# Optimization experiments

Measured on AMD Instinct MI355X. Metric: run time of the kernel, lower is better.

The kernel has to match this reference:

```python
import jax, jax.numpy as jnp
import numpy as np

EPS = 1e-5

def group_points(feat, idx):
    # feat: [B, C, N1], idx: [B, N2, K] -> [B, C, N2, K]
    return jax.vmap(lambda f, i: f[:, i])(feat, idx)

def conv_bn_relu(x, W, gamma, beta):
    # 1x1 conv2d (no bias) + training-mode BatchNorm2d + ReLU
    y = jnp.einsum('oc,bcnk->bonk', W, x)
    mean = y.mean(axis=(0, 2, 3), keepdims=True)
    var = y.var(axis=(0, 2, 3), keepdims=True)  # biased, as BN uses for normalization
    y = (y - mean) * jax.lax.rsqrt(var + EPS)
    y = y * gamma[None, :, None, None] + beta[None, :, None, None]
    return jax.nn.relu(y)

def setup_inputs() -> dict:
    key = jax.random.key(0)
    ks = jax.random.split(key, 12)
    B, N1, N2, K, C1 = 16, 4096, 1024, 32, 64
    mlp = [C1 + 3, 64, 64, 128]  # use_xyz adds 3 channels
    inp = {
        'in_xyz': jax.random.normal(ks[0], (B, 3, N1), jnp.float32),
        'out_xyz': jax.random.normal(ks[1], (B, 3, N2), jnp.float32),
        'in_feature': jax.random.normal(ks[2], (B, C1, N1), jnp.float32),
        'nbr_index': jax.random.randint(ks[3], (B, N2, K), 0, N1, jnp.int32),
    }
    for li in range(3):
        cin, cout = mlp[li], mlp[li + 1]
        inp[f'W{li}'] = jax.random.normal(ks[4 + li], (cout, cin), jnp.float32) * (1.0 / np.sqrt(cin))
        inp[f'g{li}'] = jnp.ones((cout,), jnp.float32)
        inp[f'b{li}'] = jnp.zeros((cout,), jnp.float32)
    return inp

def reference(in_xyz, out_xyz, in_feature, nbr_index,
              W0, g0, b0, W1, g1, b1, W2, g2, b2):
    # gather neighbor features: [B, C1, N2, K]
    nbr_feature = group_points(in_feature, nbr_index)
    # gather neighbor xyz, recenter on query points: [B, 3, N2, K]
    nbr_xyz = group_points(in_xyz, nbr_index) - out_xyz[:, :, :, None]
    x = jnp.concatenate([nbr_feature, nbr_xyz], axis=1)  # [B, C1+3, N2, K]
    x = conv_bn_relu(x, W0, g0, b0)
    x = conv_bn_relu(x, W1, g1, b1)
    x = conv_bn_relu(x, W2, g2, b2)
    return jnp.max(x, axis=3)  # [B, C2, N2]
```

## Files before the change

### kernel.cpp

```cpp
#include <hip/hip_runtime.h>
#include <cstdint>

typedef unsigned short u16;
typedef unsigned int   u32;
typedef __attribute__((ext_vector_type(8))) short  short8;
typedef __attribute__((ext_vector_type(4))) float  floatx4;

#define NPTS 524288

__device__ __forceinline__ float b2f(u16 h) { return __uint_as_float(((u32)h) << 16); }
__device__ __forceinline__ u16 f2b(float f) {
  u32 u = __float_as_uint(f);
  return (u16)((u + 0x7FFFu + ((u >> 16) & 1u)) >> 16);
}
__device__ __forceinline__ u32 pk_bf16(float lo, float hi) {
  return (u32)f2b(lo) | ((u32)f2b(hi) << 16);
}
__device__ __forceinline__ short8 ld_frag8(const u16* p) {
  union { uint4 q; short8 s; } x;
  x.q = *(const uint4*)p;
  return x.s;
}
__device__ __forceinline__ void bar_lds() {
  asm volatile("s_waitcnt lgkmcnt(0)\n\ts_barrier" ::: "memory");
}

__global__ __launch_bounds__(256) void prep_all(const float* __restrict__ inf,
                                                const float* __restrict__ ixyz,
                                                const float* __restrict__ W0,
                                                const float* __restrict__ W1,
                                                const float* __restrict__ W2,
                                                u16* __restrict__ featT,
                                                float4* __restrict__ xyzT,
                                                u16* __restrict__ Wb) {
  __shared__ float tile[32 * 33];
  const int bk = blockIdx.x, t = threadIdx.x;
  if (bk < 4096) {
    int b = bk >> 8, rem = bk & 255, cc = rem >> 7, nc = rem & 127;
    #pragma unroll
    for (int i = 0; i < 4; ++i) {
      int flat = t + i * 256;
      int cl = flat >> 5, nl = flat & 31;
      tile[cl * 33 + nl] = inf[(size_t)((b * 64) + cc * 32 + cl) * 4096 + nc * 32 + nl];
    }
    __syncthreads();
    #pragma unroll
    for (int i = 0; i < 4; ++i) {
      int flat = t + i * 256;
      int nl = flat >> 5, cl = flat & 31;
      featT[(size_t)((b << 12) + nc * 32 + nl) * 64 + cc * 32 + cl] = f2b(tile[cl * 33 + nl]);
    }
  } else if (bk < 4352) {
    int g = (bk - 4096) * 256 + t;
    int b = g >> 12, n = g & 4095;
    const float* p = ixyz + (size_t)b * 12288;
    xyzT[g] = make_float4(p[n], p[4096 + n], p[8192 + n], 0.f);
  } else {
    int s = (bk - 4352) * 256 + t;
    u16 v = 0;
    if (s < 6656)       { int o = s / 104, c = s % 104; if (c < 67) v = f2b(W0[o * 67 + c]); }
    else if (s < 11264) { int q = s - 6656;  int o = q / 72, c = q % 72; if (c < 64) v = f2b(W1[o * 64 + c]); }
    else                { int q = s - 11264; int o = q / 72, c = q % 72; if (c < 64) v = f2b(W2[o * 64 + c]); }
    Wb[s] = v;
  }
}

template<int KSTEPS, int OCH, bool GATHER, bool MAXOUT>
__global__ __launch_bounds__(256, 4) void gemm_layer(
    const u16* __restrict__ xsrc, const float4* __restrict__ xyzT,
    const float* __restrict__ oxyz, const int* __restrict__ nbr,
    const u16* __restrict__ Wb, const float* __restrict__ ssin,
    u16* __restrict__ yout, u32* __restrict__ gm,
    float* __restrict__ partial) {
  constexpr int PITCH = KSTEPS * 32 + 8;
  __shared__ __align__(16) u16 wsh[OCH * PITCH];
  __shared__ __align__(16) u16 xs[2][64 * PITCH];
  __shared__ float red[512];
  __shared__ float ss[GATHER ? 4 : 128];

  const int t = threadIdx.x, blk = blockIdx.x;
  const int lane = t & 63, wv = t >> 6, lr = lane & 15, quad = lane >> 4;
  const int m = t >> 2, s4 = t & 3;
  const int P0 = blk * 256;
  const int b = blk >> 7;

  {
    const u32* src = (const u32*)Wb;
    u32* dst = (u32*)wsh;
    constexpr int NW = OCH * PITCH / 2;
    #pragma unroll
    for (int i = 0; i < NW / 256; ++i) dst[t + i * 256] = src[t + i * 256];
  }
  if constexpr (!GATHER) {
    if (t < 128) ss[t] = ssin[t];
  }
  if constexpr (GATHER) {
    #pragma unroll
    for (int bu = 0; bu < 2; ++bu) {
      if (s4 == 1) {
        u16* xr = xs[bu] + m * PITCH;
        xr[67] = 0;
        #pragma unroll
        for (int j = 0; j < 9; ++j) *(uint2*)(xr + 68 + j * 4) = make_uint2(0u, 0u);
      }
    }
  }
  if constexpr (!GATHER) __syncthreads();

  int idx4[4];
  if constexpr (GATHER) {
    #pragma unroll
    for (int sub = 0; sub < 4; ++sub) idx4[sub] = nbr[P0 + sub * 64 + m];
  }

  uint4 f0, f1;
  float DX = 0.f, DY = 0.f, DZ = 0.f;

  auto issue = [&](int sub) {
    const int P = P0 + sub * 64 + m;
    if constexpr (GATHER) {
      const int id = idx4[sub];
      const u16* row = xsrc + ((size_t)((b << 12) + id)) * 64;
      f0 = *(const uint4*)(row + s4 * 16);
      f1 = *(const uint4*)(row + s4 * 16 + 8);
      if (s4 == 0) {
        const int n2 = (P & 32767) >> 5;
        float4 p = xyzT[(b << 12) + id];
        DX = p.x - oxyz[(b * 3 + 0) * 1024 + n2];
        DY = p.y - oxyz[(b * 3 + 1) * 1024 + n2];
        DZ = p.z - oxyz[(b * 3 + 2) * 1024 + n2];
      }
    } else {
      const u16* row = xsrc + ((size_t)P << 6);
      f0 = *(const uint4*)(row + s4 * 16);
      f1 = *(const uint4*)(row + s4 * 16 + 8);
    }
  };

  auto commit = [&](int bu) {
    u16* xrow = xs[bu] + m * PITCH + s4 * 16;
    if constexpr (GATHER) {
      *(uint4*)(xrow + 0) = f0;
      *(uint4*)(xrow + 8) = f1;
      if (s4 == 0) {
        u16* xr = xs[bu] + m * PITCH;
        xr[64] = f2b(DX); xr[65] = f2b(DY); xr[66] = f2b(DZ);
      }
    } else {
      u32 w[8] = { f0.x, f0.y, f0.z, f0.w, f1.x, f1.y, f1.z, f1.w };
      u32 o[8];
      #pragma unroll
      for (int i = 0; i < 8; ++i) {
        const int c = s4 * 16 + i * 2;
        float lo = fmaxf(b2f((u16)(w[i] & 0xffffu)) * ss[c]     + ss[64 + c],     0.f);
        float hi = fmaxf(b2f((u16)(w[i] >> 16))     * ss[c + 1] + ss[64 + c + 1], 0.f);
        o[i] = pk_bf16(lo, hi);
      }
      *(uint4*)(xrow + 0) = make_uint4(o[0], o[1], o[2], o[3]);
      *(uint4*)(xrow + 8) = make_uint4(o[4], o[5], o[6], o[7]);
    }
  };

  issue(0); commit(0);
  issue(1);
  __syncthreads();

  float s1[4] = {0.f, 0.f, 0.f, 0.f}, s2[4] = {0.f, 0.f, 0.f, 0.f};
  u32* yo = (u32*)yout;
  const int rg = wv >> 1, cg = wv & 1;

  for (int sub = 0; sub < 4; ++sub) {
    const int cur = sub & 1;
    if (sub < 3) commit(cur ^ 1);
    if (sub < 2) issue(sub + 2);

    if constexpr (!MAXOUT) {
      const u16* ap = xs[cur] + (wv * 16 + lr) * PITCH + quad * 8;
      const u16* bp = wsh + lr * PITCH + quad * 8;
      floatx4 acc[4];
      #pragma unroll
      for (int nt = 0; nt < 4; ++nt) acc[nt] = (floatx4){0.f, 0.f, 0.f, 0.f};
      #pragma unroll
      for (int ks = 0; ks < KSTEPS; ++ks) {
        short8 av = ld_frag8(ap + ks * 32);
        #pragma unroll
        for (int nt = 0; nt < 4; ++nt) {
          short8 bv = ld_frag8(bp + nt * 16 * PITCH + ks * 32);
          acc[nt] = __builtin_amdgcn_mfma_f32_16x16x32_bf16(av, bv, acc[nt], 0, 0, 0);
        }
      }
      const int R0 = P0 + sub * 64 + wv * 16 + quad * 4;
      #pragma unroll
      for (int nt = 0; nt < 4; ++nt) {
        #pragma unroll
        for (int r = 0; r < 4; ++r) {
          float v = acc[nt][r];
          s1[nt] += v; s2[nt] += v * v;
          float vo = __shfl_xor(v, 1);
          if ((lr & 1) == 0)
            yo[(size_t)(R0 + r) * 32 + nt * 8 + (lr >> 1)] = pk_bf16(v, vo);
        }
      }
    } else {
      const u16* bp = wsh + (cg * 64 + lr) * PITCH + quad * 8;
      short8 av[2][KSTEPS];
      #pragma unroll
      for (int h = 0; h < 2; ++h)
        #pragma unroll
        for (int ks = 0; ks < KSTEPS; ++ks)
          av[h][ks] = ld_frag8(xs[cur] + (rg * 32 + h * 16 + lr) * PITCH + quad * 8 + ks * 32);
      floatx4 acc[2][4];
      #pragma unroll
      for (int h = 0; h < 2; ++h)
        #pragma unroll
        for (int nt = 0; nt < 4; ++nt) acc[h][nt] = (floatx4){0.f, 0.f, 0.f, 0.f};
      #pragma unroll
      for (int ks = 0; ks < KSTEPS; ++ks)
        #pragma unroll
        for (int nt = 0; nt < 4; ++nt) {
          short8 bv = ld_frag8(bp + nt * 16 * PITCH + ks * 32);
          #pragma unroll
          for (int h = 0; h < 2; ++h)
            acc[h][nt] = __builtin_amdgcn_mfma_f32_16x16x32_bf16(av[h][ks], bv, acc[h][nt], 0, 0, 0);
        }
      float mx[4], mn[4];
      #pragma unroll
      for (int nt = 0; nt < 4; ++nt) {
        mx[nt] = -INFINITY; mn[nt] = INFINITY;
        #pragma unroll
        for (int h = 0; h < 2; ++h)
          #pragma unroll
          for (int r = 0; r < 4; ++r) {
            float v = acc[h][nt][r];
            s1[nt] += v; s2[nt] += v * v;
            mx[nt] = fmaxf(mx[nt], v); mn[nt] = fminf(mn[nt], v);
          }
        mx[nt] = fmaxf(mx[nt], __shfl_xor(mx[nt], 16));
        mx[nt] = fmaxf(mx[nt], __shfl_xor(mx[nt], 32));
        mn[nt] = fminf(mn[nt], __shfl_xor(mn[nt], 16));
        mn[nt] = fminf(mn[nt], __shfl_xor(mn[nt], 32));
      }
      if (lane < 16) {
        const int grp = blk * 8 + sub * 2 + rg;
        #pragma unroll
        for (int nt = 0; nt < 4; ++nt)
          gm[(size_t)grp * 128 + cg * 64 + nt * 16 + lr] = pk_bf16(mx[nt], mn[nt]);
      }
    }
    if (sub < 3) bar_lds();
  }

  #pragma unroll
  for (int nt = 0; nt < 4; ++nt) {
    s1[nt] += __shfl_xor(s1[nt], 16); s1[nt] += __shfl_xor(s1[nt], 32);
    s2[nt] += __shfl_xor(s2[nt], 16); s2[nt] += __shfl_xor(s2[nt], 32);
  }
  if (lane < 16) {
    #pragma unroll
    for (int nt = 0; nt < 4; ++nt) {
      red[wv * 64 + nt * 16 + lr] = s1[nt];
      red[256 + wv * 64 + nt * 16 + lr] = s2[nt];
    }
  }
  __syncthreads();
  if constexpr (!MAXOUT) {
    if (t < 64) {
      partial[(size_t)blk * 128 + t] = red[t] + red[64 + t] + red[128 + t] + red[192 + t];
    } else if (t < 128) {
      int c = t - 64;
      partial[(size_t)blk * 128 + t] = red[256 + c] + red[320 + c] + red[384 + c] + red[448 + c];
    }
  } else {
    if (t < 128) {
      int half = t >> 6, i = t & 63;
      partial[(size_t)blk * 256 + t] = red[half * 64 + i] + red[(half + 2) * 64 + i];
    } else {
      int c = t - 128, half = c >> 6, i = c & 63;
      partial[(size_t)blk * 256 + t] = red[256 + half * 64 + i] + red[256 + (half + 2) * 64 + i];
    }
  }
}

__global__ __launch_bounds__(256) void reduce1(const float* __restrict__ partial,
                                               float* __restrict__ tmp, int cols) {
  int c = threadIdx.x;
  if (c >= cols) return;
  int r0 = blockIdx.x * 32;
  float s = 0.f;
  for (int r = 0; r < 32; ++r) s += partial[(size_t)(r0 + r) * cols + c];
  tmp[blockIdx.x * cols + c] = s;
}

__global__ __launch_bounds__(256) void finalize2(const float* __restrict__ tmp,
                                                 const float* __restrict__ gam,
                                                 const float* __restrict__ bet,
                                                 float* __restrict__ ssout, int och) {
  __shared__ float l[256];
  int t = threadIdx.x, cols = 2 * och;
  if (t < cols) {
    float s = 0.f;
    for (int r = 0; r < 64; ++r) s += tmp[r * cols + t];
    l[t] = s;
  }
  __syncthreads();
  if (t < och) {
    const float invN = 1.f / (float)NPTS;
    float mean = l[t] * invN;
    float var  = fmaxf(l[och + t] * invN - mean * mean, 0.f);
    float scale = gam[t] * rsqrtf(var + 1e-5f);
    ssout[t] = scale;
    ssout[och + t] = bet[t] - mean * scale;
  }
}

__global__ __launch_bounds__(256) void final_out(const u32* __restrict__ gm,
                                                 const float* __restrict__ ss2,
                                                 float* __restrict__ out) {
  __shared__ float tile[64 * 33];
  int blk = blockIdx.x;
  int b = blk >> 6, rem = blk & 63, cc = rem >> 4, nn = rem & 15;
  int t = threadIdx.x;
  #pragma unroll
  for (int i = 0; i < 8; ++i) {
    int flat = t + i * 256;
    int n2l = flat >> 5, cl = flat & 31;
    int c = cc * 32 + cl;
    size_t idx = (size_t)((b << 10) + nn * 64 + n2l) * 128 + c;
    u32 p = gm[idx];
    float mx = b2f((u16)(p & 0xffffu)), mn = b2f((u16)(p >> 16));
    float scv = ss2[c], shv = ss2[128 + c];
    float v = (scv >= 0.f) ? mx : mn;
    tile[n2l * 33 + cl] = fmaxf(scv * v + shv, 0.f);
  }
  __syncthreads();
  #pragma unroll
  for (int i = 0; i < 8; ++i) {
    int flat = t + i * 256;
    int cl = flat >> 6, n2l = flat & 63;
    out[(size_t)((b * 128) + cc * 32 + cl) * 1024 + nn * 64 + n2l] = tile[n2l * 33 + cl];
  }
}

extern "C" void kernel_launch(void* const* d_in, const int* in_sizes, int n_in,
                              void* d_out, int out_size, void* d_ws, size_t ws_size,
                              hipStream_t stream) {
  const float* in_xyz  = (const float*)d_in[0];
  const float* out_xyz = (const float*)d_in[1];
  const float* in_feat = (const float*)d_in[2];
  const int*   nbr     = (const int*)d_in[3];
  const float* W0 = (const float*)d_in[4];
  const float* g0 = (const float*)d_in[5];
  const float* b0 = (const float*)d_in[6];
  const float* W1 = (const float*)d_in[7];
  const float* g1 = (const float*)d_in[8];
  const float* b1 = (const float*)d_in[9];
  const float* W2 = (const float*)d_in[10];
  const float* g2 = (const float*)d_in[11];
  const float* b2 = (const float*)d_in[12];
  float* out = (float*)d_out;

  char* ws = (char*)d_ws;
  float*  ssbuf = (float*)(ws + 0);
  u16*    Wb    = (u16*)(ws + 4096);
  float*  tmpA  = (float*)(ws + 65536);
  u16*    featT = (u16*)(ws + 262144);
  float4* xyzT  = (float4*)(ws + 8650752);
  u16*    y0    = (u16*)(ws + 9699328);
  u16*    y1    = (u16*)(ws + 76808192);
  float*  p0    = (float*)(ws + 76808192);
  float*  p1    = (float*)(ws + 262144);
  u32*    gm    = (u32*)(ws + 9699328);
  float*  p2    = (float*)(ws + 9699328 + 8388608);

  hipLaunchKernelGGL(prep_all, dim3(4432), dim3(256), 0, stream,
                     in_feat, in_xyz, W0, W1, W2, featT, xyzT, Wb);

  hipLaunchKernelGGL((gemm_layer<3, 64, true, false>), dim3(2048), dim3(256), 0, stream,
                     featT, xyzT, out_xyz, nbr, Wb, nullptr, y0, nullptr, p0);
  hipLaunchKernelGGL(reduce1, dim3(64), dim3(256), 0, stream, p0, tmpA, 128);
  hipLaunchKernelGGL(finalize2, dim3(1), dim3(256), 0, stream, tmpA, g0, b0, ssbuf, 64);

  hipLaunchKernelGGL((gemm_layer<2, 64, false, false>), dim3(2048), dim3(256), 0, stream,
                     y0, nullptr, nullptr, nullptr, Wb + 6656, ssbuf, y1, nullptr, p1);
  hipLaunchKernelGGL(reduce1, dim3(64), dim3(256), 0, stream, p1, tmpA, 128);
  hipLaunchKernelGGL(finalize2, dim3(1), dim3(256), 0, stream, tmpA, g1, b1, ssbuf + 256, 64);

  hipLaunchKernelGGL((gemm_layer<2, 128, false, true>), dim3(2048), dim3(256), 0, stream,
                     y1, nullptr, nullptr, nullptr, Wb + 11264, ssbuf + 256, nullptr, gm, p2);
  hipLaunchKernelGGL(reduce1, dim3(64), dim3(256), 0, stream, p2, tmpA, 256);
  hipLaunchKernelGGL(finalize2, dim3(1), dim3(256), 0, stream, tmpA, g2, b2, ssbuf + 512, 128);

  hipLaunchKernelGGL(final_out, dim3(1024), dim3(256), 0, stream, gm, ssbuf + 512, out);
}
```

Baseline: 205.7 us.

## Load MFMA A-fragments directly from global and fold BN stats via atomics

Removes the LDS staging double-buffer for activations: each lane now loads its A-operand fragment straight from global memory (gathered rows for layer 0, BN+ReLU applied in registers for later layers). Per-block partial statistics are replaced by atomic adds into a small set of replicated accumulators, which eliminates the separate reduce1/finalize2 kernels; each consumer kernel now computes scale/shift itself. Occupancy hints for the non-max layers are raised. The trade-off is uncoalesced per-lane fragment loads with no explicit prefetch pipelining, plus atomic contention on a few addresses and float nondeterminism.

```diff
diff --git a/kernel.cpp b/kernel.cpp
--- a/kernel.cpp
+++ b/kernel.cpp
@@ -7,6 +7,7 @@
 typedef __attribute__((ext_vector_type(4))) float  floatx4;
 
 #define NPTS 524288
+#define NREP 4
 
 __device__ __forceinline__ float b2f(u16 h) { return __uint_as_float(((u32)h) << 16); }
 __device__ __forceinline__ u16 f2b(float f) {
@@ -21,8 +22,8 @@
   x.q = *(const uint4*)p;
   return x.s;
 }
-__device__ __forceinline__ void bar_lds() {
-  asm volatile("s_waitcnt lgkmcnt(0)\n\ts_barrier" ::: "memory");
+__device__ __forceinline__ short8 u4_to_s8(uint4 q) {
+  union { uint4 q; short8 s; } x; x.q = q; return x.s;
 }
 
 __global__ __launch_bounds__(256) void prep_all(const float* __restrict__ inf,
@@ -32,7 +33,8 @@
                                                 const float* __restrict__ W2,
                                                 u16* __restrict__ featT,
                                                 float4* __restrict__ xyzT,
-                                                u16* __restrict__ Wb) {
+                                                u16* __restrict__ Wb,
+                                                float* __restrict__ gz) {
   __shared__ float tile[32 * 33];
   const int bk = blockIdx.x, t = threadIdx.x;
   if (bk < 4096) {
@@ -55,32 +57,35 @@
     int b = g >> 12, n = g & 4095;
     const float* p = ixyz + (size_t)b * 12288;
     xyzT[g] = make_float4(p[n], p[4096 + n], p[8192 + n], 0.f);
-  } else {
+  } else if (bk < 4432) {
     int s = (bk - 4352) * 256 + t;
     u16 v = 0;
     if (s < 6656)       { int o = s / 104, c = s % 104; if (c < 67) v = f2b(W0[o * 67 + c]); }
     else if (s < 11264) { int q = s - 6656;  int o = q / 72, c = q % 72; if (c < 64) v = f2b(W1[o * 64 + c]); }
     else                { int q = s - 11264; int o = q / 72, c = q % 72; if (c < 64) v = f2b(W2[o * 64 + c]); }
     Wb[s] = v;
+  } else {
+    #pragma unroll
+    for (int i = 0; i < 8; ++i) gz[t + i * 256] = 0.f;
   }
 }
 
 template<int KSTEPS, int OCH, bool GATHER, bool MAXOUT>
-__global__ __launch_bounds__(256, 4) void gemm_layer(
+__global__ __launch_bounds__(256, MAXOUT ? 4 : 5) void gemm_layer(
     const u16* __restrict__ xsrc, const float4* __restrict__ xyzT,
     const float* __restrict__ oxyz, const int* __restrict__ nbr,
-    const u16* __restrict__ Wb, const float* __restrict__ ssin,
+    const u16* __restrict__ Wb,
+    const float* __restrict__ gsin, const float* __restrict__ gam,
+    const float* __restrict__ bet,
     u16* __restrict__ yout, u32* __restrict__ gm,
-    float* __restrict__ partial) {
+    float* __restrict__ gsout) {
   constexpr int PITCH = KSTEPS * 32 + 8;
   __shared__ __align__(16) u16 wsh[OCH * PITCH];
-  __shared__ __align__(16) u16 xs[2][64 * PITCH];
   __shared__ float red[512];
   __shared__ float ss[GATHER ? 4 : 128];
 
   const int t = threadIdx.x, blk = blockIdx.x;
   const int lane = t & 63, wv = t >> 6, lr = lane & 15, quad = lane >> 4;
-  const int m = t >> 2, s4 = t & 3;
   const int P0 = blk * 256;
   const int b = blk >> 7;
 
@@ -92,106 +97,88 @@
     for (int i = 0; i < NW / 256; ++i) dst[t + i * 256] = src[t + i * 256];
   }
   if constexpr (!GATHER) {
-    if (t < 128) ss[t] = ssin[t];
-  }
-  if constexpr (GATHER) {
-    #pragma unroll
-    for (int bu = 0; bu < 2; ++bu) {
-      if (s4 == 1) {
-        u16* xr = xs[bu] + m * PITCH;
-        xr[67] = 0;
-        #pragma unroll
-        for (int j = 0; j < 9; ++j) *(uint2*)(xr + 68 + j * 4) = make_uint2(0u, 0u);
-      }
-    }
-  }
-  if constexpr (!GATHER) __syncthreads();
-
-  int idx4[4];
-  if constexpr (GATHER) {
-    #pragma unroll
-    for (int sub = 0; sub < 4; ++sub) idx4[sub] = nbr[P0 + sub * 64 + m];
-  }
-
-  uint4 f0, f1;
-  float DX = 0.f, DY = 0.f, DZ = 0.f;
-
-  auto issue = [&](int sub) {
-    const int P = P0 + sub * 64 + m;
-    if constexpr (GATHER) {
-      const int id = idx4[sub];
-      const u16* row = xsrc + ((size_t)((b << 12) + id)) * 64;
-      f0 = *(const uint4*)(row + s4 * 16);
-      f1 = *(const uint4*)(row + s4 * 16 + 8);
-      if (s4 == 0) {
-        const int n2 = (P & 32767) >> 5;
-        float4 p = xyzT[(b << 12) + id];
-        DX = p.x - oxyz[(b * 3 + 0) * 1024 + n2];
-        DY = p.y - oxyz[(b * 3 + 1) * 1024 + n2];
-        DZ = p.z - oxyz[(b * 3 + 2) * 1024 + n2];
-      }
-    } else {
-      const u16* row = xsrc + ((size_t)P << 6);
-      f0 = *(const uint4*)(row + s4 * 16);
-      f1 = *(const uint4*)(row + s4 * 16 + 8);
-    }
-  };
-
-  auto commit = [&](int bu) {
-    u16* xrow = xs[bu] + m * PITCH + s4 * 16;
-    if constexpr (GATHER) {
-      *(uint4*)(xrow + 0) = f0;
-      *(uint4*)(xrow + 8) = f1;
-      if (s4 == 0) {
-        u16* xr = xs[bu] + m * PITCH;
-        xr[64] = f2b(DX); xr[65] = f2b(DY); xr[66] = f2b(DZ);
-      }
-    } else {
-      u32 w[8] = { f0.x, f0.y, f0.z, f0.w, f1.x, f1.y, f1.z, f1.w };
-      u32 o[8];
+    if (t < 64) {
+      float a = 0.f, q = 0.f;
+      #pragma unroll
+      for (int rep = 0; rep < NREP; ++rep) {
+        a += gsin[rep * 128 + t];
+        q += gsin[rep * 128 + 64 + t];
+      }
+      const float invN = 1.f / (float)NPTS;
+      float mean = a * invN;
+      float var  = fmaxf(q * invN - mean * mean, 0.f);
+      float sc = gam[t] * rsqrtf(var + 1e-5f);
+      ss[t] = sc; ss[64 + t] = bet[t] - mean * sc;
+    }
+  }
+  __syncthreads();
+
+  float scr[2][8], shr[2][8];
+  if constexpr (!GATHER) {
+    #pragma unroll
+    for (int ks = 0; ks < 2; ++ks)
       #pragma unroll
       for (int i = 0; i < 8; ++i) {
-        const int c = s4 * 16 + i * 2;
-        float lo = fmaxf(b2f((u16)(w[i] & 0xffffu)) * ss[c]     + ss[64 + c],     0.f);
-        float hi = fmaxf(b2f((u16)(w[i] >> 16))     * ss[c + 1] + ss[64 + c + 1], 0.f);
-        o[i] = pk_bf16(lo, hi);
-      }
-      *(uint4*)(xrow + 0) = make_uint4(o[0], o[1], o[2], o[3]);
-      *(uint4*)(xrow + 8) = make_uint4(o[4], o[5], o[6], o[7]);
-    }
-  };
-
-  issue(0); commit(0);
-  issue(1);
-  __syncthreads();
+        const int c = ks * 32 + quad * 8 + i;
+        scr[ks][i] = ss[c]; shr[ks][i] = ss[64 + c];
+      }
+  }
 
   float s1[4] = {0.f, 0.f, 0.f, 0.f}, s2[4] = {0.f, 0.f, 0.f, 0.f};
   u32* yo = (u32*)yout;
-  const int rg = wv >> 1, cg = wv & 1;
-
-  for (int sub = 0; sub < 4; ++sub) {
-    const int cur = sub & 1;
-    if (sub < 3) commit(cur ^ 1);
-    if (sub < 2) issue(sub + 2);
-
-    if constexpr (!MAXOUT) {
-      const u16* ap = xs[cur] + (wv * 16 + lr) * PITCH + quad * 8;
-      const u16* bp = wsh + lr * PITCH + quad * 8;
+
+  if constexpr (!MAXOUT) {
+    const u16* bp = wsh + lr * PITCH + quad * 8;
+    #pragma unroll
+    for (int sub = 0; sub < 4; ++sub) {
+      const int R = P0 + sub * 64 + wv * 16 + lr;
+      short8 av[KSTEPS];
+      if constexpr (GATHER) {
+        const int id = nbr[R];
+        const u16* row = xsrc + (size_t)((b << 12) + id) * 64;
+        uint4 a0 = *(const uint4*)(row + quad * 8);
+        uint4 a1 = *(const uint4*)(row + quad * 8 + 32);
+        u32 w0 = 0u, w1 = 0u;
+        if (quad == 0) {
+          const int n2 = (R & 32767) >> 5;
+          float4 p = xyzT[(b << 12) + id];
+          float dx = p.x - oxyz[(b * 3 + 0) * 1024 + n2];
+          float dy = p.y - oxyz[(b * 3 + 1) * 1024 + n2];
+          float dz = p.z - oxyz[(b * 3 + 2) * 1024 + n2];
+          w0 = pk_bf16(dx, dy); w1 = (u32)f2b(dz);
+        }
+        av[0] = u4_to_s8(a0);
+        av[1] = u4_to_s8(a1);
+        av[2] = u4_to_s8(make_uint4(w0, w1, 0u, 0u));
+      } else {
+        const u16* row = xsrc + ((size_t)R << 6);
+        #pragma unroll
+        for (int ks = 0; ks < KSTEPS; ++ks) {
+          uint4 raw = *(const uint4*)(row + ks * 32 + quad * 8);
+          u32 w[4] = { raw.x, raw.y, raw.z, raw.w };
+          u32 o[4];
+          #pragma unroll
+          for (int j = 0; j < 4; ++j) {
+            float lo = fmaxf(b2f((u16)(w[j] & 0xffffu)) * scr[ks][2 * j]     + shr[ks][2 * j],     0.f);
+            float hi = fmaxf(b2f((u16)(w[j] >> 16))     * scr[ks][2 * j + 1] + shr[ks][2 * j + 1], 0.f);
+            o[j] = pk_bf16(lo, hi);
+          }
+          av[ks] = u4_to_s8(make_uint4(o[0], o[1], o[2], o[3]));
+        }
+      }
       floatx4 acc[4];
       #pragma unroll
       for (int nt = 0; nt < 4; ++nt) acc[nt] = (floatx4){0.f, 0.f, 0.f, 0.f};
       #pragma unroll
-      for (int ks = 0; ks < KSTEPS; ++ks) {
-        short8 av = ld_frag8(ap + ks * 32);
+      for (int ks = 0; ks < KSTEPS; ++ks)
         #pragma unroll
         for (int nt = 0; nt < 4; ++nt) {
           short8 bv = ld_frag8(bp + nt * 16 * PITCH + ks * 32);
-          acc[nt] = __builtin_amdgcn_mfma_f32_16x16x32_bf16(av, bv, acc[nt], 0, 0, 0);
-        }
-      }
+          acc[nt] = __builtin_amdgcn_mfma_f32_16x16x32_bf16(av[ks], bv, acc[nt], 0, 0, 0);
+        }
       const int R0 = P0 + sub * 64 + wv * 16 + quad * 4;
       #pragma unroll
-      for (int nt = 0; nt < 4; ++nt) {
+      for (int nt = 0; nt < 4; ++nt)
         #pragma unroll
         for (int r = 0; r < 4; ++r) {
           float v = acc[nt][r];
@@ -200,22 +187,37 @@
           if ((lr & 1) == 0)
             yo[(size_t)(R0 + r) * 32 + nt * 8 + (lr >> 1)] = pk_bf16(v, vo);
         }
-      }
-    } else {
-      const u16* bp = wsh + (cg * 64 + lr) * PITCH + quad * 8;
-      short8 av[2][KSTEPS];
+    }
+  } else {
+    const int rg = wv >> 1, cg = wv & 1;
+    const u16* bp = wsh + (cg * 64 + lr) * PITCH + quad * 8;
+    for (int sub = 0; sub < 4; ++sub) {
+      short8 av[2][2];
+      #pragma unroll
+      for (int h = 0; h < 2; ++h) {
+        const int R = P0 + sub * 64 + rg * 32 + h * 16 + lr;
+        const u16* row = xsrc + ((size_t)R << 6);
+        #pragma unroll
+        for (int ks = 0; ks < 2; ++ks) {
+          uint4 raw = *(const uint4*)(row + ks * 32 + quad * 8);
+          u32 w[4] = { raw.x, raw.y, raw.z, raw.w };
+          u32 o[4];
+          #pragma unroll
+          for (int j = 0; j < 4; ++j) {
+            float lo = fmaxf(b2f((u16)(w[j] & 0xffffu)) * scr[ks][2 * j]     + shr[ks][2 * j],     0.f);
+            float hi = fmaxf(b2f((u16)(w[j] >> 16))     * scr[ks][2 * j + 1] + shr[ks][2 * j + 1], 0.f);
+            o[j] = pk_bf16(lo, hi);
+          }
+          av[h][ks] = u4_to_s8(make_uint4(o[0], o[1], o[2], o[3]));
+        }
+      }
+      floatx4 acc[2][4];
       #pragma unroll
       for (int h = 0; h < 2; ++h)
         #pragma unroll
-        for (int ks = 0; ks < KSTEPS; ++ks)
-          av[h][ks] = ld_frag8(xs[cur] + (rg * 32 + h * 16 + lr) * PITCH + quad * 8 + ks * 32);
-      floatx4 acc[2][4];
-      #pragma unroll
-      for (int h = 0; h < 2; ++h)
-        #pragma unroll
         for (int nt = 0; nt < 4; ++nt) acc[h][nt] = (floatx4){0.f, 0.f, 0.f, 0.f};
       #pragma unroll
-      for (int ks = 0; ks < KSTEPS; ++ks)
+      for (int ks = 0; ks < 2; ++ks)
         #pragma unroll
         for (int nt = 0; nt < 4; ++nt) {
           short8 bv = ld_frag8(bp + nt * 16 * PITCH + ks * 32);
@@ -247,7 +249,6 @@
           gm[(size_t)grp * 128 + cg * 64 + nt * 16 + lr] = pk_bf16(mx[nt], mn[nt]);
       }
     }
-    if (sub < 3) bar_lds();
   }
 
   #pragma unroll
@@ -263,63 +264,49 @@
     }
   }
   __syncthreads();
+  float* gb = gsout + (blk & (NREP - 1)) * (MAXOUT ? 256 : 128);
   if constexpr (!MAXOUT) {
     if (t < 64) {
-      partial[(size_t)blk * 128 + t] = red[t] + red[64 + t] + red[128 + t] + red[192 + t];
+      unsafeAtomicAdd(&gb[t], red[t] + red[64 + t] + red[128 + t] + red[192 + t]);
     } else if (t < 128) {
       int c = t - 64;
-      partial[(size_t)blk * 128 + t] = red[256 + c] + red[320 + c] + red[384 + c] + red[448 + c];
+      unsafeAtomicAdd(&gb[64 + c], red[256 + c] + red[320 + c] + red[384 + c] + red[448 + c]);
     }
   } else {
     if (t < 128) {
       int half = t >> 6, i = t & 63;
-      partial[(size_t)blk * 256 + t] = red[half * 64 + i] + red[(half + 2) * 64 + i];
+      unsafeAtomicAdd(&gb[t], red[half * 64 + i] + red[(half + 2) * 64 + i]);
     } else {
       int c = t - 128, half = c >> 6, i = c & 63;
-      partial[(size_t)blk * 256 + t] = red[256 + half * 64 + i] + red[256 + (half + 2) * 64 + i];
-    }
-  }
-}
-
-__global__ __launch_bounds__(256) void reduce1(const float* __restrict__ partial,
-                                               float* __restrict__ tmp, int cols) {
-  int c = threadIdx.x;
-  if (c >= cols) return;
-  int r0 = blockIdx.x * 32;
-  float s = 0.f;
-  for (int r = 0; r < 32; ++r) s += partial[(size_t)(r0 + r) * cols + c];
-  tmp[blockIdx.x * cols + c] = s;
-}
-
-__global__ __launch_bounds__(256) void finalize2(const float* __restrict__ tmp,
+      unsafeAtomicAdd(&gb[128 + c], red[256 + half * 64 + i] + red[256 + (half + 2) * 64 + i]);
+    }
+  }
+}
+
+__global__ __launch_bounds__(256) void final_out(const u32* __restrict__ gm,
+                                                 const float* __restrict__ gs,
                                                  const float* __restrict__ gam,
                                                  const float* __restrict__ bet,
-                                                 float* __restrict__ ssout, int och) {
-  __shared__ float l[256];
-  int t = threadIdx.x, cols = 2 * och;
-  if (t < cols) {
-    float s = 0.f;
-    for (int r = 0; r < 64; ++r) s += tmp[r * cols + t];
-    l[t] = s;
-  }
-  __syncthreads();
-  if (t < och) {
-    const float invN = 1.f / (float)NPTS;
-    float mean = l[t] * invN;
-    float var  = fmaxf(l[och + t] * invN - mean * mean, 0.f);
-    float scale = gam[t] * rsqrtf(var + 1e-5f);
-    ssout[t] = scale;
-    ssout[och + t] = bet[t] - mean * scale;
-  }
-}
-
-__global__ __launch_bounds__(256) void final_out(const u32* __restrict__ gm,
-                                                 const float* __restrict__ ss2,
                                                  float* __restrict__ out) {
   __shared__ float tile[64 * 33];
+  __shared__ float ssc[128], ssh[128];
   int blk = blockIdx.x;
   int b = blk >> 6, rem = blk & 63, cc = rem >> 4, nn = rem & 15;
   int t = threadIdx.x;
+  if (t < 128) {
+    float a = 0.f, q = 0.f;
+    #pragma unroll
+    for (int rep = 0; rep < NREP; ++rep) {
+      a += gs[rep * 256 + t];
+      q += gs[rep * 256 + 128 + t];
+    }
+    const float invN = 1.f / (float)NPTS;
+    float mean = a * invN;
+    float var  = fmaxf(q * invN - mean * mean, 0.f);
+    float sc = gam[t] * rsqrtf(var + 1e-5f);
+    ssc[t] = sc; ssh[t] = bet[t] - mean * sc;
+  }
+  __syncthreads();
   #pragma unroll
   for (int i = 0; i < 8; ++i) {
     int flat = t + i * 256;
@@ -327,9 +314,9 @@
     int c = cc * 32 + cl;
     size_t idx = (size_t)((b << 10) + nn * 64 + n2l) * 128 + c;
     u32 p = gm[idx];
-    float mx = b2f((u16)(p & 0xffffu)), mn = b2f((u16)(p >> 16));
-    float scv = ss2[c], shv = ss2[128 + c];
-    float v = (scv >= 0.f) ? mx : mn;
+    float mxv = b2f((u16)(p & 0xffffu)), mnv = b2f((u16)(p >> 16));
+    float scv = ssc[c], shv = ssh[c];
+    float v = (scv >= 0.f) ? mxv : mnv;
     tile[n2l * 33 + cl] = fmaxf(scv * v + shv, 0.f);
   }
   __syncthreads();
@@ -360,35 +347,30 @@
   float* out = (float*)d_out;
 
   char* ws = (char*)d_ws;
-  float*  ssbuf = (float*)(ws + 0);
   u16*    Wb    = (u16*)(ws + 4096);
-  float*  tmpA  = (float*)(ws + 65536);
+  float*  gs0   = (float*)(ws + 49152);
+  float*  gs1   = (float*)(ws + 51200);
+  float*  gs2   = (float*)(ws + 53248);
   u16*    featT = (u16*)(ws + 262144);
   float4* xyzT  = (float4*)(ws + 8650752);
   u16*    y0    = (u16*)(ws + 9699328);
   u16*    y1    = (u16*)(ws + 76808192);
-  float*  p0    = (float*)(ws + 76808192);
-  float*  p1    = (float*)(ws + 262144);
   u32*    gm    = (u32*)(ws + 9699328);
-  float*  p2    = (float*)(ws + 9699328 + 8388608);
-
-  hipLaunchKernelGGL(prep_all, dim3(4432), dim3(256), 0, stream,
-                     in_feat, in_xyz, W0, W1, W2, featT, xyzT, Wb);
+
+  hipLaunchKernelGGL(prep_all, dim3(4433), dim3(256), 0, stream,
+                     in_feat, in_xyz, W0, W1, W2, featT, xyzT, Wb, gs0);
 
   hipLaunchKernelGGL((gemm_layer<3, 64, true, false>), dim3(2048), dim3(256), 0, stream,
-                     featT, xyzT, out_xyz, nbr, Wb, nullptr, y0, nullptr, p0);
-  hipLaunchKernelGGL(reduce1, dim3(64), dim3(256), 0, stream, p0, tmpA, 128);
-  hipLaunchKernelGGL(finalize2, dim3(1), dim3(256), 0, stream, tmpA, g0, b0, ssbuf, 64);
+                     featT, xyzT, out_xyz, nbr, Wb, nullptr, nullptr, nullptr,
+                     y0, nullptr, gs0);
 
   hipLaunchKernelGGL((gemm_layer<2, 64, false, false>), dim3(2048), dim3(256), 0, stream,
-                     y0, nullptr, nullptr, nullptr, Wb + 6656, ssbuf, y1, nullptr, p1);
-  hipLaunchKernelGGL(reduce1, dim3(64), dim3(256), 0, stream, p1, tmpA, 128);
-  hipLaunchKernelGGL(finalize2, dim3(1), dim3(256), 0, stream, tmpA, g1, b1, ssbuf + 256, 64);
+                     y0, nullptr, nullptr, nullptr, Wb + 6656, gs0, g0, b0,
+                     y1, nullptr, gs1);
 
   hipLaunchKernelGGL((gemm_layer<2, 128, false, true>), dim3(2048), dim3(256), 0, stream,
-                     y1, nullptr, nullptr, nullptr, Wb + 11264, ssbuf + 256, nullptr, gm, p2);
-  hipLaunchKernelGGL(reduce1, dim3(64), dim3(256), 0, stream, p2, tmpA, 256);
-  hipLaunchKernelGGL(finalize2, dim3(1), dim3(256), 0, stream, tmpA, g2, b2, ssbuf + 512, 128);
-
-  hipLaunchKernelGGL(final_out, dim3(1024), dim3(256), 0, stream, gm, ssbuf + 512, out);
-}
+                     y1, nullptr, nullptr, nullptr, Wb + 11264, gs1, g1, b1,
+                     nullptr, gm, gs2);
+
+  hipLaunchKernelGGL(final_out, dim3(1024), dim3(256), 0, stream, gm, gs2, g2, b2, out);
+}
```

After: 226.8 us. 10.3% more time.
